# Optimization experiments

Hardware: AMD Instinct MI355X
Metric: run time of the kernel (lower is better)

Reference implementation:

```python
import jax, jax.numpy as jnp
import numpy as np
from jax import lax

B, D, H, N = 2048, 256, 256, 64  # batch, input_dim, hidden_dim, n_slots
F = 2 * D + 1                    # feat_dim = input_dim*2 + 1


def setup_inputs() -> dict:
    key = jax.random.key(0)
    ks = jax.random.split(key, 12)
    s = 0.05
    return {
        "x_t": jax.random.normal(ks[0], (B, D), jnp.float32),
        "h_mem_prev": jnp.zeros((B, H), jnp.float32),
        "slots": jax.random.normal(ks[1], (B, N, D), jnp.float32),
        "cum_feats": jax.random.normal(ks[2], (B, N, D), jnp.float32),
        "delta_t": jax.random.uniform(ks[3], (B, N), jnp.float32),
        "filled": jax.random.randint(ks[4], (B, N), 0, 2) > 0,
        # nn.Linear weights (out, in) convention
        "Wq": jax.random.normal(ks[5], (H, D), jnp.float32) * s,
        "Wk": jax.random.normal(ks[6], (H, D), jnp.float32) * s,
        "Wv": jax.random.normal(ks[7], (D, D), jnp.float32) * s,
        "bv": jax.random.normal(ks[8], (D,), jnp.float32) * s,
        # nn.LSTM params, gate order [i, f, g, o]
        "W_ih": jax.random.normal(ks[9], (4 * H, F), jnp.float32) * s,
        "W_hh": jax.random.normal(ks[10], (4 * H, H), jnp.float32) * s,
        "b_ih": jax.random.normal(ks[11], (4 * H,), jnp.float32) * s,
        "b_hh": jnp.zeros((4 * H,), jnp.float32),
    }


def _lstm_last(seq, W_ih, W_hh, b_ih, b_hh):
    """seq: (B, T, F) -> last hidden output (B, H). PyTorch gate order i,f,g,o."""
    Bsz = seq.shape[0]
    Hh = W_hh.shape[1]
    b = b_ih + b_hh

    def step(carry, x_t):
        h, c = carry
        z = x_t @ W_ih.T + h @ W_hh.T + b  # (B, 4H)
        i, f, g, o = jnp.split(z, 4, axis=-1)
        c = jax.nn.sigmoid(f) * c + jax.nn.sigmoid(i) * jnp.tanh(g)
        h = jax.nn.sigmoid(o) * jnp.tanh(c)
        return (h, c), None

    init = (jnp.zeros((Bsz, Hh), seq.dtype), jnp.zeros((Bsz, Hh), seq.dtype))
    (h, _), _ = lax.scan(step, init, jnp.swapaxes(seq, 0, 1))
    return h


def reference(x_t, h_mem_prev, slots, cum_feats, delta_t, filled,
              Wq, Wk, Wv, bv, W_ih, W_hh, b_ih, b_hh):
    Bsz = x_t.shape[0]
    delta_t = delta_t + 1.0
    cum_feats = cum_feats + x_t[:, None, :]

    q = x_t @ Wq.T                          # (B, H)
    keys = jnp.einsum('bnd,hd->bnh', slots, Wk)
    sims = jnp.einsum('bnh,bh->bn', keys, q)

    v = x_t @ Wv.T + bv                     # (B, D)

    empty = ~filled
    empty_any = empty.any(axis=1)
    idx_empty = jnp.argmax(empty.astype(jnp.float32), axis=1)
    idx_cont = jnp.argmax(sims, axis=1)
    idx = jnp.where(empty_any, idx_empty, idx_cont)  # (B,) int

    ar = jnp.arange(Bsz)
    slots = slots.at[ar, idx].set(v)
    cum_feats = cum_feats.at[ar, idx].set(x_t)
    delta_t = delta_t.at[ar, idx].set(0.0)
    filled = filled.at[ar, idx].set(True)

    mem_seq = jnp.concatenate([slots, cum_feats, delta_t[..., None]], axis=2)  # (B, N, F)
    h_mem = _lstm_last(mem_seq, W_ih, W_hh, b_ih, b_hh)
    return h_mem, slots, cum_feats, delta_t, filled
```

## Files before the change

### kernel.cpp

```cpp
#include <hip/hip_runtime.h>
#include <hip/hip_bf16.h>
#include <cstdint>
#include <cstddef>


typedef short s16x8 __attribute__((ext_vector_type(8)));
typedef float f32x4 __attribute__((ext_vector_type(4)));
typedef int   i32x4 __attribute__((ext_vector_type(4)));
typedef unsigned short u16x4 __attribute__((ext_vector_type(4)));

static __device__ __forceinline__ unsigned short f2b(float f){
  union{float f; unsigned int u;} v; v.f = f;
  unsigned int r = v.u + 0x7fffu + ((v.u >> 16) & 1u);
  return (unsigned short)(r >> 16);
}
static __device__ __forceinline__ float b2f(unsigned short h){
  union{unsigned int u; float f;} v; v.u = ((unsigned int)h) << 16; return v.f;
}
static __device__ __forceinline__ unsigned int pack2(float a, float b){
  return (unsigned int)f2b(a) | ((unsigned int)f2b(b) << 16);
}
static __device__ __forceinline__ float fsig(float x){ return 1.0f / (1.0f + __expf(-x)); }
static __device__ __forceinline__ float ftanh(float x){ return 2.0f / (1.0f + __expf(-2.0f * x)) - 1.0f; }
static __device__ __forceinline__ float wred(float p){
  p += __shfl_down(p, 32); p += __shfl_down(p, 16); p += __shfl_down(p, 8);
  p += __shfl_down(p, 4);  p += __shfl_down(p, 2);  p += __shfl_down(p, 1);
  return p;
}
static __device__ __forceinline__ void gload16(const void* g, void* lds){
  __builtin_amdgcn_global_load_lds(
      (const __attribute__((address_space(1))) unsigned int*)g,
      (__attribute__((address_space(3))) unsigned int*)lds, 16, 0, 0);
}

#define WSCALE (0.30f / 127.0f)

__global__ __launch_bounds__(256) void k_prep(
    const float* __restrict__ wih, const float* __restrict__ whh,
    const float* __restrict__ bih, const float* __restrict__ bhh,
    unsigned short* __restrict__ wfB, signed char* __restrict__ wfrag8,
    float* __restrict__ bias, float* __restrict__ wlast){
  int id = blockIdx.x * 256 + threadIdx.x;
  {
    int frag = id >> 9;
    int l = (id >> 3) & 63;
    int j = id & 7;
    int kt = frag >> 6, ct = frag & 63;
    int col = ct * 16 + (l & 15);
    int k   = kt * 32 + (l >> 4) * 8 + j;
    wfB[id] = f2b(wih[col * 513 + k]);
  }
  if (id < 262144){
    int frag = id >> 10;
    int lane = (id >> 4) & 63;
    int j    = id & 15;
    int w   = frag >> 5;
    int kt2 = (frag >> 3) & 3;
    int nt  = frag & 7;
    int g   = nt >> 1, hh = nt & 1;
    int colg = g * 256 + w * 32 + hh * 16 + (lane & 15);
    int k    = kt2 * 64 + (lane >> 4) * 16 + j;
    int q = __float2int_rn(whh[colg * 256 + k] * (1.0f / WSCALE));
    q = q > 127 ? 127 : (q < -127 ? -127 : q);
    wfrag8[id] = (signed char)q;
  }
  if (id < 1024){
    bias[id]  = bih[id] + bhh[id];
    wlast[id] = wih[id * 513 + 512];
  }
}

__global__ __launch_bounds__(256) void k_route(
    const float* __restrict__ x, const float* __restrict__ slots,
    const float* __restrict__ delta, const int* __restrict__ filled,
    const float* __restrict__ Wq, const float* __restrict__ Wk,
    const float* __restrict__ Wv, const float* __restrict__ bv,
    int* __restrict__ idx_ws, float* __restrict__ v_ws,
    float* __restrict__ delta_out, float* __restrict__ filled_out){
  int b = blockIdx.x, tid = threadIdx.x, l = tid & 63, w = tid >> 6;
  __shared__ float xs[256], qs[256], qks[256], sims[64];
  __shared__ int sidx;
  xs[tid] = x[b * 256 + tid];
  if (tid < 64){
    unsigned long long em = __ballot(filled[b * 64 + tid] == 0);
    if (tid == 0) sidx = em ? (int)__builtin_ctzll(em) : -1;
  }
  __syncthreads();
  for (int t = 0; t < 64; ++t){
    int h = w * 64 + t;
    float pv = 0.f;
    #pragma unroll
    for (int j2 = 0; j2 < 4; ++j2)
      pv += Wv[h * 256 + l + 64 * j2] * xs[l + 64 * j2];
    pv = wred(pv);
    if (l == 0) v_ws[b * 256 + h] = pv + bv[h];
  }
  if (sidx < 0){
    for (int t = 0; t < 64; ++t){
      int h = w * 64 + t;
      float p = 0.f;
      #pragma unroll
      for (int j2 = 0; j2 < 4; ++j2)
        p += Wq[h * 256 + l + 64 * j2] * xs[l + 64 * j2];
      p = wred(p);
      if (l == 0) qs[h] = p;
    }
    __syncthreads();
    {
      int d = tid; float p = 0.f;
      for (int h = 0; h < 256; ++h) p += qs[h] * Wk[h * 256 + d];
      qks[d] = p;
    }
    __syncthreads();
    for (int t = 0; t < 16; ++t){
      int n = w * 16 + t;
      float p = 0.f;
      #pragma unroll
      for (int j2 = 0; j2 < 4; ++j2)
        p += slots[(size_t)(b * 64 + n) * 256 + l + 64 * j2] * qks[l + 64 * j2];
      p = wred(p);
      if (l == 0) sims[n] = p;
    }
    __syncthreads();
    if (tid == 0){
      int ic = 0; float best = sims[0];
      for (int n = 1; n < 64; ++n) if (sims[n] > best){ best = sims[n]; ic = n; }
      sidx = ic;
    }
  }
  __syncthreads();
  int id = sidx;
  if (tid == 0) idx_ws[b] = id;
  if (tid < 64){
    int n = tid; bool sel = (n == id);
    delta_out[b * 64 + n]  = sel ? 0.0f : (delta[b * 64 + n] + 1.0f);
    filled_out[b * 64 + n] = (sel || filled[b * 64 + n] != 0) ? 1.0f : 0.0f;
  }
}

__global__ __launch_bounds__(512) void k_scatter(
    const float* __restrict__ x, const float* __restrict__ slots,
    const float* __restrict__ cum, const int* __restrict__ idx_ws,
    const float* __restrict__ v_ws,
    float* __restrict__ slots_out, float* __restrict__ cum_out,
    unsigned short* __restrict__ abf){
  int rg = threadIdx.x >> 6, l = threadIdx.x & 63;
  int row = blockIdx.x * 8 + rg;
  int b = row >> 6, n = row & 63;
  bool sel = (n == idx_ws[b]);
  float4 f0, f1;
  if (l < 32){
    int k0 = l * 8;
    const float* src = sel ? (v_ws + (size_t)b * 256 + k0)
                           : (slots + (size_t)row * 256 + k0);
    f0 = ((const float4*)src)[0]; f1 = ((const float4*)src)[1];
    float4* d = (float4*)(slots_out + (size_t)row * 256 + k0);
    d[0] = f0; d[1] = f1;
  } else {
    int k0 = (l - 32) * 8;
    const float4* xp = (const float4*)(x + (size_t)b * 256 + k0);
    float4 x0 = xp[0], x1 = xp[1];
    if (sel){ f0 = x0; f1 = x1; }
    else {
      const float4* cp = (const float4*)(cum + (size_t)row * 256 + k0);
      f0 = cp[0]; f1 = cp[1];
      f0.x += x0.x; f0.y += x0.y; f0.z += x0.z; f0.w += x0.w;
      f1.x += x1.x; f1.y += x1.y; f1.z += x1.z; f1.w += x1.w;
    }
    float4* d = (float4*)(cum_out + (size_t)row * 256 + k0);
    d[0] = f0; d[1] = f1;
  }
  uint4 q;
  q.x = pack2(f0.x, f0.y); q.y = pack2(f0.z, f0.w);
  q.z = pack2(f1.x, f1.y); q.w = pack2(f1.z, f1.w);
  *(uint4*)(abf + (size_t)row * 512 + l * 8) = q;
}

__global__ __launch_bounds__(512) void k_gemm(
    const unsigned short* __restrict__ abf,
    const float* __restrict__ dlt,
    const unsigned short* __restrict__ wfB,
    const float* __restrict__ wlast, const float* __restrict__ bias,
    unsigned short* __restrict__ z0){
  extern __shared__ unsigned char L[];
  int tid = threadIdx.x, l = tid & 63, w = tid >> 6;
  int bid = blockIdx.x;
  int gw = (bid & 7) * 512 + (bid >> 3);
  int n_idx = gw & 3, m_idx = gw >> 2;
  int m0 = m_idx * 128, n0 = n_idx * 256, bA = m0 >> 6;
  int wm = w & 1, wn = w >> 1;
  int cl = l & 15, lhi = l >> 4;

  auto stageA = [&](int kt, int abase){
    const unsigned short* s = abf + (size_t)(m0 + (w & 1) * 64 + l) * 512
                              + kt * 32 + (w >> 1) * 8;
    gload16(s, L + abase + (w >> 1) * 2048 + (w & 1) * 1024);
  };
  auto stageB = [&](int kt, int bbase){
    const unsigned short* s = wfB + ((size_t)(kt * 64 + n_idx * 16 + w * 2)) * 512 + l * 8;
    gload16(s,       L + bbase + (w * 2) * 1024);
    gload16(s + 512, L + bbase + (w * 2) * 1024 + 1024);
  };

  f32x4 acc[4][4];
  #pragma unroll
  for (int mi = 0; mi < 4; ++mi)
    #pragma unroll
    for (int ni = 0; ni < 4; ++ni){ f32x4 zr = {0.f,0.f,0.f,0.f}; acc[mi][ni] = zr; }

  stageA(0, 0);      stageB(0, 24576);
  stageA(1, 8192);   stageB(1, 24576 + 16384);

  #pragma unroll
  for (int kt = 0; kt < 16; ++kt){
    if (kt < 15) asm volatile("s_waitcnt vmcnt(3)" ::: "memory");
    else         asm volatile("s_waitcnt vmcnt(0)" ::: "memory");
    __builtin_amdgcn_s_barrier();
    __builtin_amdgcn_sched_barrier(0);
    if (kt < 14){
      int nb = (kt + 2) % 3;
      stageA(kt + 2, nb * 8192);
      stageB(kt + 2, 24576 + nb * 16384);
    }
    int ab = (kt % 3) * 8192, bb = 24576 + (kt % 3) * 16384;
    s16x8 a[4], bf[4];
    #pragma unroll
    for (int mi = 0; mi < 4; ++mi)
      a[mi] = *(const s16x8*)(L + ab + lhi * 2048 + (wm * 64 + mi * 16 + cl) * 16);
    #pragma unroll
    for (int ni = 0; ni < 4; ++ni)
      bf[ni] = *(const s16x8*)(L + bb + (wn * 4 + ni) * 1024 + l * 16);
    #pragma unroll
    for (int ni = 0; ni < 4; ++ni)
      #pragma unroll
      for (int mi = 0; mi < 4; ++mi)
        acc[mi][ni] = __builtin_amdgcn_mfma_f32_16x16x32_bf16(a[mi], bf[ni], acc[mi][ni], 0, 0, 0);
  }
  __syncthreads();

  float dv[4][4];
  #pragma unroll
  for (int mi = 0; mi < 4; ++mi)
    #pragma unroll
    for (int reg = 0; reg < 4; ++reg)
      dv[mi][reg] = dlt[(bA + wm) * 64 + mi * 16 + lhi * 4 + reg];
  #pragma unroll
  for (int mi = 0; mi < 4; ++mi)
    #pragma unroll
    for (int reg = 0; reg < 4; ++reg){
      int row = wm * 64 + mi * 16 + lhi * 4 + reg;
      #pragma unroll
      for (int ni = 0; ni < 4; ++ni){
        int col = wn * 64 + ni * 16 + cl;
        int gc = n0 + col;
        float val = acc[mi][ni][reg] + dv[mi][reg] * wlast[gc] + bias[gc];
        *(unsigned short*)(L + row * 512 + ((col * 2) ^ ((row & 7) << 4))) = f2b(val);
      }
    }
  __syncthreads();
  #pragma unroll
  for (int rr = 0; rr < 8; ++rr){
    int id = rr * 512 + tid;
    int row = id >> 5, cs = id & 31;
    int bq = bA + (row >> 6), nq = row & 63;
    uint4 v = *(const uint4*)(L + row * 512 + ((cs * 16) ^ ((row & 7) << 4)));
    *(uint4*)(z0 + ((size_t)nq * 2048 + bq) * 1024 + n0 + cs * 8) = v;
  }
}

__global__ __launch_bounds__(512) void k_lstm(
    const unsigned short* __restrict__ z0,
    const signed char* __restrict__ wfrag8,
    float* __restrict__ hm){
  extern __shared__ unsigned char smem[];
  float* zhhf = (float*)smem;
  unsigned char* hbf = smem + 32768;
  int tid = threadIdx.x, l = tid & 63, w = tid >> 6;
  int cl = l & 15, lhi = l >> 4;
  int b0 = blockIdx.x * 8;
  int rr_o = tid >> 6;
  int chb  = (tid & 63) * 4;
  int hoff = rr_o * 256 + ((chb & ~15) ^ ((rr_o & 7) << 4)) + (chb & 15);

  for (int i = tid; i < 1024; i += 512) ((unsigned int*)hbf)[i] = 0u;

  i32x4 wpin[32];
  #pragma unroll
  for (int f = 0; f < 32; ++f)
    wpin[f] = *(const i32x4*)(wfrag8 + ((size_t)w * 32 + f) * 1024 + l * 16);

  float cst[4];
  #pragma unroll
  for (int i = 0; i < 4; ++i) cst[i] = 0.f;
  const float s_comb = WSCALE / 127.0f;
  __syncthreads();

  for (int n = 0; n < 64; ++n){
    u16x4 zg[4];
    {
      const unsigned short* zr = z0 + ((size_t)n * 2048 + b0 + rr_o) * 1024 + chb;
      zg[0] = *(const u16x4*)(zr);
      zg[1] = *(const u16x4*)(zr + 256);
      zg[2] = *(const u16x4*)(zr + 512);
      zg[3] = *(const u16x4*)(zr + 768);
    }
    i32x4 acc[8];
    #pragma unroll
    for (int nt = 0; nt < 8; ++nt){ i32x4 zr4 = {0, 0, 0, 0}; acc[nt] = zr4; }
    #pragma unroll
    for (int kt2 = 0; kt2 < 4; ++kt2){
      i32x4 a = *(const i32x4*)(hbf + cl * 256 +
                 ((kt2 * 64 + lhi * 16) ^ ((cl & 7) << 4)));
      #pragma unroll
      for (int nt = 0; nt < 8; ++nt)
        acc[nt] = __builtin_amdgcn_mfma_i32_16x16x64_i8(a, wpin[kt2 * 8 + nt], acc[nt], 0, 0, 0);
    }
    if (l < 32){
      #pragma unroll
      for (int hh = 0; hh < 2; ++hh){
        int ch = w * 32 + hh * 16 + cl;
        #pragma unroll
        for (int reg = 0; reg < 4; ++reg){
          int rr = lhi * 4 + reg;
          zhhf[0 * 2048 + rr * 256 + ch] = (float)acc[0 + hh][reg];
          zhhf[1 * 2048 + rr * 256 + ch] = (float)acc[2 + hh][reg];
          zhhf[2 * 2048 + rr * 256 + ch] = (float)acc[4 + hh][reg];
          zhhf[3 * 2048 + rr * 256 + ch] = (float)acc[6 + hh][reg];
        }
      }
    }
    __syncthreads();
    f32x4 p[4];
    #pragma unroll
    for (int g = 0; g < 4; ++g)
      p[g] = *(const f32x4*)(zhhf + g * 2048 + rr_o * 256 + chb);
    unsigned int hw = 0;
    #pragma unroll
    for (int i = 0; i < 4; ++i){
      float zi  = fmaf(p[0][i], s_comb, b2f(zg[0][i]));
      float zf  = fmaf(p[1][i], s_comb, b2f(zg[1][i]));
      float zgv = fmaf(p[2][i], s_comb, b2f(zg[2][i]));
      float zo  = fmaf(p[3][i], s_comb, b2f(zg[3][i]));
      float cv = fsig(zf) * cst[i] + fsig(zi) * ftanh(zgv);
      cst[i] = cv;
      float hv = fsig(zo) * ftanh(cv);
      unsigned int q = (unsigned int)(__float2int_rn(hv * 127.0f) & 255);
      hw |= q << (8 * i);
      if (n == 63) hm[(size_t)(b0 + rr_o) * 256 + chb + i] = hv;
    }
    *(unsigned int*)(hbf + hoff) = hw;
    __syncthreads();
  }
}

extern "C" void kernel_launch(void* const* d_in, const int* in_sizes, int n_in,
                              void* d_out, int out_size, void* d_ws, size_t ws_size,
                              hipStream_t stream){
  const float* x      = (const float*)d_in[0];
  const float* slots  = (const float*)d_in[2];
  const float* cum    = (const float*)d_in[3];
  const float* delta  = (const float*)d_in[4];
  const int*   filled = (const int*)d_in[5];
  const float* Wq  = (const float*)d_in[6];
  const float* Wk  = (const float*)d_in[7];
  const float* Wv  = (const float*)d_in[8];
  const float* bv  = (const float*)d_in[9];
  const float* wih = (const float*)d_in[10];
  const float* whh = (const float*)d_in[11];
  const float* bih = (const float*)d_in[12];
  const float* bhh = (const float*)d_in[13];

  float* out        = (float*)d_out;
  float* hm         = out;
  float* slots_out  = out + 524288;
  float* cum_out    = out + 34078720;
  float* delta_out  = out + 67633152;
  float* filled_out = out + 67764224;

  char* ws = (char*)d_ws;
  int*            idx_ws  = (int*)ws;
  float*          v_ws    = (float*)(ws + 8192);
  float*          bias    = (float*)(ws + 2105344);
  float*          wlast   = (float*)(ws + 2109440);
  unsigned short* wfB     = (unsigned short*)(ws + 2113536);
  signed char*    wfrag8  = (signed char*)(ws + 3162112);
  unsigned short* abf     = (unsigned short*)(ws + 3686400);
  unsigned short* z0      = (unsigned short*)(ws + 3686400 + 134217728);

  k_prep<<<dim3(2048), dim3(256), 0, stream>>>(wih, whh, bih, bhh, wfB, wfrag8, bias, wlast);
  k_route<<<dim3(2048), dim3(256), 0, stream>>>(x, slots, delta, filled, Wq, Wk, Wv, bv,
                                                idx_ws, v_ws, delta_out, filled_out);
  k_scatter<<<dim3(16384), dim3(512), 0, stream>>>(x, slots, cum, idx_ws, v_ws,
                                                   slots_out, cum_out, abf);
  k_gemm<<<dim3(4096), dim3(512), 73728, stream>>>(abf, delta_out,
                                                   wfB, wlast, bias, z0);
  k_lstm<<<dim3(256), dim3(512), 36864, stream>>>(z0, wfrag8, hm);
}
```

Before: 519.3 us.

## Merge weight prep into route kernel and prefetch next LSTM step's gate inputs

The weight conversion work (bf16 W_ih fragments, int8 W_hh fragments, bias and last-column extraction) now runs in extra blocks of the routing kernel, which removes one kernel launch and lets the two independent jobs run concurrently. The LSTM loop is unrolled by two with double-buffered registers so each step issues the global loads of the precomputed input-projection values for the next timestep before its MFMA and activation work. This hides global latency on the serial recurrence at the cost of a few more registers in a kernel that already pins 32 weight fragments.

```diff
diff --git a/kernel.cpp b/kernel.cpp
--- a/kernel.cpp
+++ b/kernel.cpp
@@ -35,49 +35,50 @@
 
 #define WSCALE (0.30f / 127.0f)
 
-__global__ __launch_bounds__(256) void k_prep(
-    const float* __restrict__ wih, const float* __restrict__ whh,
-    const float* __restrict__ bih, const float* __restrict__ bhh,
-    unsigned short* __restrict__ wfB, signed char* __restrict__ wfrag8,
-    float* __restrict__ bias, float* __restrict__ wlast){
-  int id = blockIdx.x * 256 + threadIdx.x;
-  {
-    int frag = id >> 9;
-    int l = (id >> 3) & 63;
-    int j = id & 7;
-    int kt = frag >> 6, ct = frag & 63;
-    int col = ct * 16 + (l & 15);
-    int k   = kt * 32 + (l >> 4) * 8 + j;
-    wfB[id] = f2b(wih[col * 513 + k]);
-  }
-  if (id < 262144){
-    int frag = id >> 10;
-    int lane = (id >> 4) & 63;
-    int j    = id & 15;
-    int w   = frag >> 5;
-    int kt2 = (frag >> 3) & 3;
-    int nt  = frag & 7;
-    int g   = nt >> 1, hh = nt & 1;
-    int colg = g * 256 + w * 32 + hh * 16 + (lane & 15);
-    int k    = kt2 * 64 + (lane >> 4) * 16 + j;
-    int q = __float2int_rn(whh[colg * 256 + k] * (1.0f / WSCALE));
-    q = q > 127 ? 127 : (q < -127 ? -127 : q);
-    wfrag8[id] = (signed char)q;
-  }
-  if (id < 1024){
-    bias[id]  = bih[id] + bhh[id];
-    wlast[id] = wih[id * 513 + 512];
-  }
-}
-
 __global__ __launch_bounds__(256) void k_route(
     const float* __restrict__ x, const float* __restrict__ slots,
     const float* __restrict__ delta, const int* __restrict__ filled,
     const float* __restrict__ Wq, const float* __restrict__ Wk,
     const float* __restrict__ Wv, const float* __restrict__ bv,
+    const float* __restrict__ wih, const float* __restrict__ whh,
+    const float* __restrict__ bih, const float* __restrict__ bhh,
     int* __restrict__ idx_ws, float* __restrict__ v_ws,
-    float* __restrict__ delta_out, float* __restrict__ filled_out){
-  int b = blockIdx.x, tid = threadIdx.x, l = tid & 63, w = tid >> 6;
+    float* __restrict__ delta_out, float* __restrict__ filled_out,
+    unsigned short* __restrict__ wfB, signed char* __restrict__ wfrag8,
+    float* __restrict__ bias, float* __restrict__ wlast){
+  int tid = threadIdx.x;
+  if (blockIdx.x >= 2048){
+    int id = (blockIdx.x - 2048) * 256 + tid;
+    {
+      int frag = id >> 9;
+      int l = (id >> 3) & 63;
+      int j = id & 7;
+      int kt = frag >> 6, ct = frag & 63;
+      int col = ct * 16 + (l & 15);
+      int k   = kt * 32 + (l >> 4) * 8 + j;
+      wfB[id] = f2b(wih[col * 513 + k]);
+    }
+    if (id < 262144){
+      int frag = id >> 10;
+      int lane = (id >> 4) & 63;
+      int j    = id & 15;
+      int w   = frag >> 5;
+      int kt2 = (frag >> 3) & 3;
+      int nt  = frag & 7;
+      int g   = nt >> 1, hh = nt & 1;
+      int colg = g * 256 + w * 32 + hh * 16 + (lane & 15);
+      int k    = kt2 * 64 + (lane >> 4) * 16 + j;
+      int q = __float2int_rn(whh[colg * 256 + k] * (1.0f / WSCALE));
+      q = q > 127 ? 127 : (q < -127 ? -127 : q);
+      wfrag8[id] = (signed char)q;
+    }
+    if (id < 1024){
+      bias[id]  = bih[id] + bhh[id];
+      wlast[id] = wih[id * 513 + 512];
+    }
+    return;
+  }
+  int b = blockIdx.x, l = tid & 63, w = tid >> 6;
   __shared__ float xs[256], qs[256], qks[256], sims[64];
   __shared__ int sidx;
   xs[tid] = x[b * 256 + tid];
@@ -281,6 +282,7 @@
   int rr_o = tid >> 6;
   int chb  = (tid & 63) * 4;
   int hoff = rr_o * 256 + ((chb & ~15) ^ ((rr_o & 7) << 4)) + (chb & 15);
+  const unsigned short* zbase = z0 + (size_t)(b0 + rr_o) * 1024 + chb;
 
   for (int i = tid; i < 1024; i += 512) ((unsigned int*)hbf)[i] = 0u;
 
@@ -295,62 +297,78 @@
   const float s_comb = WSCALE / 127.0f;
   __syncthreads();
 
-  for (int n = 0; n < 64; ++n){
-    u16x4 zg[4];
-    {
-      const unsigned short* zr = z0 + ((size_t)n * 2048 + b0 + rr_o) * 1024 + chb;
-      zg[0] = *(const u16x4*)(zr);
-      zg[1] = *(const u16x4*)(zr + 256);
-      zg[2] = *(const u16x4*)(zr + 512);
-      zg[3] = *(const u16x4*)(zr + 768);
-    }
-    i32x4 acc[8];
-    #pragma unroll
-    for (int nt = 0; nt < 8; ++nt){ i32x4 zr4 = {0, 0, 0, 0}; acc[nt] = zr4; }
-    #pragma unroll
-    for (int kt2 = 0; kt2 < 4; ++kt2){
-      i32x4 a = *(const i32x4*)(hbf + cl * 256 +
-                 ((kt2 * 64 + lhi * 16) ^ ((cl & 7) << 4)));
-      #pragma unroll
-      for (int nt = 0; nt < 8; ++nt)
-        acc[nt] = __builtin_amdgcn_mfma_i32_16x16x64_i8(a, wpin[kt2 * 8 + nt], acc[nt], 0, 0, 0);
-    }
-    if (l < 32){
-      #pragma unroll
-      for (int hh = 0; hh < 2; ++hh){
-        int ch = w * 32 + hh * 16 + cl;
-        #pragma unroll
-        for (int reg = 0; reg < 4; ++reg){
-          int rr = lhi * 4 + reg;
-          zhhf[0 * 2048 + rr * 256 + ch] = (float)acc[0 + hh][reg];
-          zhhf[1 * 2048 + rr * 256 + ch] = (float)acc[2 + hh][reg];
-          zhhf[2 * 2048 + rr * 256 + ch] = (float)acc[4 + hh][reg];
-          zhhf[3 * 2048 + rr * 256 + ch] = (float)acc[6 + hh][reg];
-        }
-      }
-    }
-    __syncthreads();
-    f32x4 p[4];
-    #pragma unroll
-    for (int g = 0; g < 4; ++g)
-      p[g] = *(const f32x4*)(zhhf + g * 2048 + rr_o * 256 + chb);
-    unsigned int hw = 0;
-    #pragma unroll
-    for (int i = 0; i < 4; ++i){
-      float zi  = fmaf(p[0][i], s_comb, b2f(zg[0][i]));
-      float zf  = fmaf(p[1][i], s_comb, b2f(zg[1][i]));
-      float zgv = fmaf(p[2][i], s_comb, b2f(zg[2][i]));
-      float zo  = fmaf(p[3][i], s_comb, b2f(zg[3][i]));
-      float cv = fsig(zf) * cst[i] + fsig(zi) * ftanh(zgv);
-      cst[i] = cv;
-      float hv = fsig(zo) * ftanh(cv);
-      unsigned int q = (unsigned int)(__float2int_rn(hv * 127.0f) & 255);
-      hw |= q << (8 * i);
-      if (n == 63) hm[(size_t)(b0 + rr_o) * 256 + chb + i] = hv;
-    }
-    *(unsigned int*)(hbf + hoff) = hw;
-    __syncthreads();
-  }
+  u16x4 zgA[4], zgB[4];
+  {
+    const unsigned short* zr = zbase;
+    zgA[0] = *(const u16x4*)(zr);
+    zgA[1] = *(const u16x4*)(zr + 256);
+    zgA[2] = *(const u16x4*)(zr + 512);
+    zgA[3] = *(const u16x4*)(zr + 768);
+  }
+
+  #define LSTM_STEP(NVAL, ZGCUR, ZGNXT, NXT_OFF)                               \
+  {                                                                            \
+    int n = (NVAL);                                                            \
+    if (n + (NXT_OFF) < 64){                                                   \
+      const unsigned short* zr = zbase + (size_t)(n + (NXT_OFF)) * 2097152;    \
+      ZGNXT[0] = *(const u16x4*)(zr);                                          \
+      ZGNXT[1] = *(const u16x4*)(zr + 256);                                    \
+      ZGNXT[2] = *(const u16x4*)(zr + 512);                                    \
+      ZGNXT[3] = *(const u16x4*)(zr + 768);                                    \
+    }                                                                          \
+    i32x4 acc[8];                                                              \
+    _Pragma("unroll")                                                          \
+    for (int nt = 0; nt < 8; ++nt){ i32x4 zr4 = {0, 0, 0, 0}; acc[nt] = zr4; } \
+    _Pragma("unroll")                                                          \
+    for (int kt2 = 0; kt2 < 4; ++kt2){                                         \
+      i32x4 a = *(const i32x4*)(hbf + cl * 256 +                               \
+                 ((kt2 * 64 + lhi * 16) ^ ((cl & 7) << 4)));                   \
+      _Pragma("unroll")                                                        \
+      for (int nt = 0; nt < 8; ++nt)                                           \
+        acc[nt] = __builtin_amdgcn_mfma_i32_16x16x64_i8(a, wpin[kt2 * 8 + nt], acc[nt], 0, 0, 0); \
+    }                                                                          \
+    if (l < 32){                                                               \
+      _Pragma("unroll")                                                        \
+      for (int hh = 0; hh < 2; ++hh){                                          \
+        int ch = w * 32 + hh * 16 + cl;                                        \
+        _Pragma("unroll")                                                      \
+        for (int reg = 0; reg < 4; ++reg){                                     \
+          int rr = lhi * 4 + reg;                                              \
+          zhhf[0 * 2048 + rr * 256 + ch] = (float)acc[0 + hh][reg];            \
+          zhhf[1 * 2048 + rr * 256 + ch] = (float)acc[2 + hh][reg];            \
+          zhhf[2 * 2048 + rr * 256 + ch] = (float)acc[4 + hh][reg];            \
+          zhhf[3 * 2048 + rr * 256 + ch] = (float)acc[6 + hh][reg];            \
+        }                                                                      \
+      }                                                                        \
+    }                                                                          \
+    __syncthreads();                                                           \
+    f32x4 p[4];                                                                \
+    _Pragma("unroll")                                                          \
+    for (int g = 0; g < 4; ++g)                                                \
+      p[g] = *(const f32x4*)(zhhf + g * 2048 + rr_o * 256 + chb);              \
+    unsigned int hw = 0;                                                       \
+    _Pragma("unroll")                                                          \
+    for (int i = 0; i < 4; ++i){                                               \
+      float zi  = fmaf(p[0][i], s_comb, b2f(ZGCUR[0][i]));                     \
+      float zf  = fmaf(p[1][i], s_comb, b2f(ZGCUR[1][i]));                     \
+      float zgv = fmaf(p[2][i], s_comb, b2f(ZGCUR[2][i]));                     \
+      float zo  = fmaf(p[3][i], s_comb, b2f(ZGCUR[3][i]));                     \
+      float cv = fsig(zf) * cst[i] + fsig(zi) * ftanh(zgv);                    \
+      cst[i] = cv;                                                             \
+      float hv = fsig(zo) * ftanh(cv);                                         \
+      unsigned int q = (unsigned int)(__float2int_rn(hv * 127.0f) & 255);      \
+      hw |= q << (8 * i);                                                      \
+      if (n == 63) hm[(size_t)(b0 + rr_o) * 256 + chb + i] = hv;               \
+    }                                                                          \
+    *(unsigned int*)(hbf + hoff) = hw;                                         \
+    __syncthreads();                                                           \
+  }
+
+  for (int n2 = 0; n2 < 64; n2 += 2){
+    LSTM_STEP(n2,     zgA, zgB, 1)
+    LSTM_STEP(n2 + 1, zgB, zgA, 1)
+  }
+  #undef LSTM_STEP
 }
 
 extern "C" void kernel_launch(void* const* d_in, const int* in_sizes, int n_in,
@@ -387,9 +405,11 @@
   unsigned short* abf     = (unsigned short*)(ws + 3686400);
   unsigned short* z0      = (unsigned short*)(ws + 3686400 + 134217728);
 
-  k_prep<<<dim3(2048), dim3(256), 0, stream>>>(wih, whh, bih, bhh, wfB, wfrag8, bias, wlast);
-  k_route<<<dim3(2048), dim3(256), 0, stream>>>(x, slots, delta, filled, Wq, Wk, Wv, bv,
-                                                idx_ws, v_ws, delta_out, filled_out);
+  k_route<<<dim3(4096), dim3(256), 0, stream>>>(x, slots, delta, filled,
+                                                Wq, Wk, Wv, bv,
+                                                wih, whh, bih, bhh,
+                                                idx_ws, v_ws, delta_out, filled_out,
+                                                wfB, wfrag8, bias, wlast);
   k_scatter<<<dim3(16384), dim3(512), 0, stream>>>(x, slots, cum, idx_ws, v_ws,
                                                    slots_out, cum_out, abf);
   k_gemm<<<dim3(4096), dim3(512), 73728, stream>>>(abf, delta_out,
```

Result: no change. 517.0 us, median of 2 (-0.4%).
